# Kernel tuning notes

Measured on AMD Instinct MI355X. Metric: run time of the kernel, lower is better.

Reference implementation:

```python
import jax, jax.numpy as jnp
import numpy as np

B, L, D_MODEL, N_HEADS = 2, 2048, 2048, 16
HEAD_DIM = D_MODEL // N_HEADS
EPS = 1e-6
ROPE_THETA = 10000.0


def rms_norm(x, scale):
    # normalize over head_dim, learnable per-dim scale (QKNorm)
    var = jnp.mean(jnp.square(x), axis=-1, keepdims=True)
    return x * jax.lax.rsqrt(var + EPS) * scale


def rope(x, offset=0):
    # x: [B, H, T, D]; rotate-half rotary embedding over flattened positions
    T, D = x.shape[-2], x.shape[-1]
    half = D // 2
    inv_freq = 1.0 / (ROPE_THETA ** (jnp.arange(0, half, dtype=jnp.float32) / half))
    pos = jnp.arange(T, dtype=jnp.float32) + offset
    ang = pos[:, None] * inv_freq[None, :]            # [T, half]
    cos, sin = jnp.cos(ang), jnp.sin(ang)
    x1, x2 = x[..., :half], x[..., half:]
    return jnp.concatenate([x1 * cos - x2 * sin, x1 * sin + x2 * cos], axis=-1)


def setup_inputs() -> dict:
    key = jax.random.key(0)
    ks = jax.random.split(key, 7)
    s = 1.0 / np.sqrt(D_MODEL)
    x = jax.random.normal(ks[0], (B, L, D_MODEL), dtype=jnp.float32)
    w_qkv = jax.random.uniform(ks[1], (D_MODEL, 3 * D_MODEL), jnp.float32, -s, s)
    b_qkv = jax.random.uniform(ks[2], (3 * D_MODEL,), jnp.float32, -s, s)
    q_scale = jnp.ones((HEAD_DIM,), jnp.float32)
    k_scale = jnp.ones((HEAD_DIM,), jnp.float32)
    w_out = jax.random.uniform(ks[3], (D_MODEL, D_MODEL), jnp.float32, -s, s)
    b_out = jax.random.uniform(ks[4], (D_MODEL,), jnp.float32, -s, s)
    mask = jnp.tril(jnp.ones((L, L), dtype=bool))   # causal block mask pattern
    return {"x": x, "w_qkv": w_qkv, "b_qkv": b_qkv, "q_scale": q_scale,
            "k_scale": k_scale, "w_out": w_out, "b_out": b_out, "mask": mask}


def reference(x, w_qkv, b_qkv, q_scale, k_scale, w_out, b_out, mask):
    b, t, _ = x.shape
    qkv = x @ w_qkv + b_qkv                                   # [B, T, 3*D]
    qkv = qkv.reshape(b, t, 3, N_HEADS, HEAD_DIM)
    q, k, v = jnp.moveaxis(qkv, 2, 0)                          # each [B, T, H, D]
    q = jnp.transpose(q, (0, 2, 1, 3))                         # [B, H, T, D]
    k = jnp.transpose(k, (0, 2, 1, 3))
    v = jnp.transpose(v, (0, 2, 1, 3))
    q = rms_norm(q, q_scale)
    k = rms_norm(k, k_scale)
    q = rope(q, offset=0)
    k = rope(k, offset=0)
    scores = jnp.einsum('bhqd,bhkd->bhqk', q, k) / np.sqrt(HEAD_DIM)
    scores = jnp.where(mask[None, None, :, :], scores, jnp.float32(-1e30))
    attn = jax.nn.softmax(scores, axis=-1)
    out = jnp.einsum('bhqk,bhkd->bhqd', attn, v)               # [B, H, T, D]
    out = jnp.transpose(out, (0, 2, 1, 3)).reshape(b, t, D_MODEL)
    return out @ w_out + b_out
```

## Files before the change

### kernel.cpp

```cpp
#include <hip/hip_runtime.h>
#include <hip/hip_bf16.h>
#include <stdint.h>


typedef unsigned short ushort8 __attribute__((ext_vector_type(8)));
typedef unsigned short ushort4v __attribute__((ext_vector_type(4)));
typedef short          bf16x8 __attribute__((ext_vector_type(8)));
typedef float          f32x4  __attribute__((ext_vector_type(4)));

#define B_   2
#define L_   2048
#define DM   2048
#define NH   16
#define HD   128
#define QKW  4096

__device__ __forceinline__ uint16_t f2bf(float f){
  uint32_t u = __builtin_bit_cast(uint32_t, f);
  u += 0x7FFFu + ((u >> 16) & 1u);
  return (uint16_t)(u >> 16);
}
__device__ __forceinline__ float bf2f(uint16_t h){
  uint32_t u = ((uint32_t)h) << 16;
  return __builtin_bit_cast(float, u);
}

#define GLD16(gp, lp) __builtin_amdgcn_global_load_lds( \
  (const __attribute__((address_space(1))) void*)(gp),  \
  (__attribute__((address_space(3))) void*)(lp), 16, 0, 0)

__global__ __launch_bounds__(256) void prep(
    const float* __restrict__ Wqkv, uint16_t* __restrict__ WqkvT,
    const float* __restrict__ Wout, uint16_t* __restrict__ WoutT,
    const float* __restrict__ x, uint16_t* __restrict__ xb,
    float* __restrict__ ct, float* __restrict__ st)
{
  __shared__ float T[64][65];
  const int bid = blockIdx.x;
  const int tid = threadIdx.x;

  if (bid < 4096){
    const float* W; uint16_t* Wt; int R = 2048, C; int rb, cb;
    if (bid < 3072){ W = Wqkv; Wt = WqkvT; C = 6144; rb = bid & 31; cb = bid >> 5; }
    else           { int i = bid - 3072; W = Wout; Wt = WoutT; C = 2048; rb = i & 31; cb = i >> 5; }
#pragma unroll
    for (int i=0;i<4;i++){
      int rr = i*16 + (tid >> 4);
      int cc = (tid & 15) * 4;
      float4 v = *(const float4*)(W + (size_t)(rb*64 + rr) * C + cb*64 + cc);
      T[rr][cc] = v.x; T[rr][cc+1] = v.y; T[rr][cc+2] = v.z; T[rr][cc+3] = v.w;
    }
    __syncthreads();
    const int oc = tid >> 2, rc = (tid & 3) * 16;
    ushort8 o0, o1;
#pragma unroll
    for (int j=0;j<8;j++){ o0[j] = f2bf(T[rc+j][oc]); o1[j] = f2bf(T[rc+8+j][oc]); }
    size_t ob = (size_t)(cb*64 + oc) * R + rb*64 + rc;
    *(ushort8*)(Wt + ob)     = o0;
    *(ushort8*)(Wt + ob + 8) = o1;
  } else if (bid < 8192){
    int i = (bid - 4096) * 256 + tid;
    const float4* xv = (const float4*)x;
    float4 a = xv[(size_t)i*2], b = xv[(size_t)i*2+1];
    ushort8 v;
    v[0]=f2bf(a.x); v[1]=f2bf(a.y); v[2]=f2bf(a.z); v[3]=f2bf(a.w);
    v[4]=f2bf(b.x); v[5]=f2bf(b.y); v[6]=f2bf(b.z); v[7]=f2bf(b.w);
    *(ushort8*)(xb + (size_t)i*8) = v;
  } else {
    int i = (bid - 8192) * 256 + tid;
    int t = i >> 6, d = i & 63;
    float invf = powf(10000.f, -(float)d * (1.f/64.f));
    float s, c;
    sincosf((float)t * invf, &s, &c);
    ct[i] = c; st[i] = s;
  }
}

template<int MODE>
__global__ __launch_bounds__(512, 2) void gemm8p(
    const uint16_t* __restrict__ A, const uint16_t* __restrict__ Bt,
    const float* __restrict__ bias, void* __restrict__ Cv, void* __restrict__ Cv2,
    int M, int N, int K, int nbn, int ldc,
    const float* __restrict__ qs, const float* __restrict__ ks,
    const float* __restrict__ ct, const float* __restrict__ st)
{
  __shared__ uint16_t LA[3*16384];
  __shared__ uint16_t LB[3*8192];
  __shared__ float sums[4][2][64];
  const int nwg = (M >> 8) * nbn;
  const int q8  = nwg >> 3;
  const int id  = ((int)blockIdx.x & 7) * q8 + ((int)blockIdx.x >> 3);
  const int bm = id / nbn, bn = id % nbn;
  const int tid = threadIdx.x;
  const int lane = tid & 63, w = tid >> 6;
  const int wm = w & 3, wn = w >> 2;
  const int l15 = lane & 15, lh = lane >> 4;
  const int NT = K >> 6;

  const int qs3 = ((lane & 7) ^ ((lane >> 3) & 7)) * 8;
  const uint16_t* gA_ = A  + (size_t)((bm << 8) + (w << 5) + (lane >> 3)) * K + qs3;
  const uint16_t* gB_ = Bt + (size_t)((bn << 7) + (w << 4) + (lane >> 3)) * K + qs3;
  uint16_t* lA_ = LA + (w << 11);
  uint16_t* lB_ = LB + (w << 10);

  const int sw0 = ((lh       ^ (l15 & 7)) << 3);
  const int sw1 = (((4 | lh) ^ (l15 & 7)) << 3);
  const int aoff = (((wm << 6) + l15) << 6);
  const int boff = (((wn << 5) + l15) << 6);
  const int bno[4] = {0, 1024, 4096, 5120};

  f32x4 acc[4][4];
#pragma unroll
  for (int i=0;i<4;i++)
#pragma unroll
    for (int j=0;j<4;j++) acc[i][j] = f32x4{0.f,0.f,0.f,0.f};

  auto STAGE_A = [&](int tt, int s, int i){
    GLD16(gA_ + (size_t)tt*64 + (size_t)(i*8)*K, lA_ + s*16384 + i*512);
  };
  auto STAGE_B = [&](int tt, int s, int i){
    GLD16(gB_ + (size_t)tt*64 + (size_t)(i*8)*K, lB_ + s*8192 + i*512);
  };

#pragma unroll
  for (int i=0;i<4;i++) STAGE_A(0, 0, i);
#pragma unroll
  for (int i=0;i<2;i++) STAGE_B(0, 0, i);
#pragma unroll
  for (int i=0;i<4;i++) STAGE_A(1, 1, i);
#pragma unroll
  for (int i=0;i<2;i++) STAGE_B(1, 1, i);
  asm volatile("s_waitcnt vmcnt(6)" ::: "memory");
  __builtin_amdgcn_s_barrier();

  int sl = 0, sl2 = 2;
  for (int t = 0; t < NT; ++t){
    const bool pf = (t + 2 < NT);
    const uint16_t* la = LA + sl*16384;
    const uint16_t* lb = LB + sl*8192;

    bf16x8 af0[4], bf0[4], af1[4], bf1[4];
#pragma unroll
    for (int mi=0;mi<4;mi++) af0[mi] = *(const bf16x8*)(la + aoff + mi*1024 + sw0);
#pragma unroll
    for (int ni=0;ni<4;ni++) bf0[ni] = *(const bf16x8*)(lb + boff + bno[ni] + sw0);
#pragma unroll
    for (int mi=0;mi<4;mi++) af1[mi] = *(const bf16x8*)(la + aoff + mi*1024 + sw1);
#pragma unroll
    for (int ni=0;ni<4;ni++) bf1[ni] = *(const bf16x8*)(lb + boff + bno[ni] + sw1);
    if (pf){
      STAGE_A(t+2, sl2, 0); STAGE_A(t+2, sl2, 1);
      STAGE_A(t+2, sl2, 2); STAGE_A(t+2, sl2, 3);
      STAGE_B(t+2, sl2, 0); STAGE_B(t+2, sl2, 1);
    }
    __builtin_amdgcn_s_setprio(1);
#pragma unroll
    for (int mi=0;mi<4;mi++)
#pragma unroll
      for (int ni=0;ni<4;ni++)
        acc[mi][ni] = __builtin_amdgcn_mfma_f32_16x16x32_bf16(af0[mi], bf0[ni], acc[mi][ni], 0, 0, 0);
#pragma unroll
    for (int mi=0;mi<4;mi++)
#pragma unroll
      for (int ni=0;ni<4;ni++)
        acc[mi][ni] = __builtin_amdgcn_mfma_f32_16x16x32_bf16(af1[mi], bf1[ni], acc[mi][ni], 0, 0, 0);
    __builtin_amdgcn_s_setprio(0);

    if (t < NT-2)       { asm volatile("s_waitcnt vmcnt(6)" ::: "memory"); }
    else if (t == NT-2) { asm volatile("s_waitcnt vmcnt(0)" ::: "memory"); }
    if (t < NT-1) __builtin_amdgcn_s_barrier();
    sl  = (sl  == 2) ? 0 : sl  + 1;
    sl2 = (sl2 == 2) ? 0 : sl2 + 1;
  }

  const int cm = (bm << 8) + (wm << 6);
  const int cn = (bn << 7);
  int dc[4];
#pragma unroll
  for (int ni=0;ni<4;ni++) dc[ni] = (wn<<5) + ((ni>>1)<<6) + ((ni&1)<<4) + l15;
  float bs[4];
#pragma unroll
  for (int ni=0;ni<4;ni++) bs[ni] = bias[cn + dc[ni]];

  if (MODE == 0){
#pragma unroll
    for (int mi=0;mi<4;mi++)
#pragma unroll
      for (int r=0;r<4;r++){
        int rowg = cm + mi*16 + lh*4 + r;
#pragma unroll
        for (int ni=0;ni<4;ni++)
          ((float*)Cv)[(size_t)rowg * ldc + cn + dc[ni]] = acc[mi][ni][r] + bs[ni];
      }
  } else {
    const int part = bn >> 4;
    if (part == 2){
      uint16_t* vtp = (uint16_t*)Cv2;
      const int h  = bn & 15;
      const int bb = cm >> 11;
      const int t0 = (cm & (L_-1)) + lh*4;
#pragma unroll
      for (int mi=0;mi<4;mi++){
#pragma unroll
        for (int ni=0;ni<4;ni++){
          ushort4v pk;
#pragma unroll
          for (int r=0;r<4;r++) pk[r] = f2bf(acc[mi][ni][r] + bs[ni]);
          *(ushort4v*)(vtp + ((size_t)((bb*16 + h)*128 + dc[ni]))*L_ + t0 + mi*16) = pk;
        }
      }
    } else {
      uint16_t* Cb = (uint16_t*)Cv;
      const float* scp = part ? ks : qs;
      float scv[4];
#pragma unroll
      for (int ni=0;ni<4;ni++) scv[ni] = scp[dc[ni]];
      float ssum[4][4];
#pragma unroll
      for (int mi=0;mi<4;mi++)
#pragma unroll
        for (int r=0;r<4;r++){
          float s = 0.f;
#pragma unroll
          for (int ni=0;ni<4;ni++){
            float v = acc[mi][ni][r] + bs[ni];
            acc[mi][ni][r] = v;
            s += v*v;
          }
          s += __shfl_xor(s, 1); s += __shfl_xor(s, 2);
          s += __shfl_xor(s, 4); s += __shfl_xor(s, 8);
          ssum[mi][r] = s;
        }
      if (l15 == 0){
#pragma unroll
        for (int mi=0;mi<4;mi++)
#pragma unroll
          for (int r=0;r<4;r++) sums[wm][wn][mi*16 + lh*4 + r] = ssum[mi][r];
      }
      __syncthreads();
      const int dd0 = (wn<<5) + l15, dd1 = dd0 + 16;
#pragma unroll
      for (int mi=0;mi<4;mi++){
#pragma unroll
        for (int r=0;r<4;r++){
          int rid = mi*16 + lh*4 + r;
          float tot = ssum[mi][r] + sums[wm][wn^1][rid];
          float iv = rsqrtf(tot * 0.0078125f + 1e-6f);
          int rowg = cm + rid;
          int t = rowg & (L_-1);
          float y0 = acc[mi][0][r] * iv * scv[0];
          float y1 = acc[mi][1][r] * iv * scv[1];
          float y2 = acc[mi][2][r] * iv * scv[2];
          float y3 = acc[mi][3][r] * iv * scv[3];
          float c0 = ct[t*64 + dd0], s0 = st[t*64 + dd0];
          float c1 = ct[t*64 + dd1], s1 = st[t*64 + dd1];
          size_t rb_ = (size_t)rowg * ldc + cn;
          Cb[rb_ + dc[0]] = f2bf(y0*c0 - y2*s0);
          Cb[rb_ + dc[1]] = f2bf(y1*c1 - y3*s1);
          Cb[rb_ + dc[2]] = f2bf(y0*s0 + y2*c0);
          Cb[rb_ + dc[3]] = f2bf(y1*s1 + y3*c1);
        }
      }
    }
  }
}

__global__ __launch_bounds__(256) void flash_attn(
    const uint16_t* __restrict__ qk, const uint16_t* __restrict__ vt,
    uint16_t* __restrict__ ao)
{
  const int bh = blockIdx.x;
  const int qp = blockIdx.y;
  const int b = bh >> 4, h = bh & 15;
  const int tid = threadIdx.x;
  const int lane = tid & 63, w = tid >> 6;
  const int l15 = lane & 15, lh = lane >> 4;

  __shared__ uint16_t Ks[64][136];
  __shared__ uint16_t Vs[128][72];
  __shared__ uint16_t Ps[4][16][72];

  const float SCL = 0.12751744f;

  for (int sel = 0; sel < 2; sel++){
    const int qb = sel ? (31 - qp) : qp;

    const size_t qrow = (size_t)b * L_ + qb*64 + w*16 + l15;
    const uint16_t* qp_ = qk + qrow * QKW + h * HD;
    bf16x8 qf[4];
#pragma unroll
    for (int c = 0; c < 4; c++) qf[c] = *(const bf16x8*)(qp_ + c*32 + lh*8);

    float m_s = -3.0e38f, l_s = 0.f;
    f32x4 oacc[8];
#pragma unroll
    for (int nt = 0; nt < 8; nt++) oacc[nt] = f32x4{0.f,0.f,0.f,0.f};

    const int ntile = qb + 1;
    ushort8 rk[4], rv[4];

#pragma unroll
    for (int i = 0; i < 4; i++){
      int g = i*256 + tid, row = g >> 4, c = g & 15;
      rk[i] = *(const ushort8*)(qk + ((size_t)b*L_ + row)*QKW + DM + h*HD + c*8);
    }
#pragma unroll
    for (int i = 0; i < 4; i++){
      int g = i*256 + tid, d = g >> 3, c = g & 7;
      rv[i] = *(const ushort8*)(vt + ((size_t)bh*HD + d)*L_ + c*8);
    }

    for (int kt = 0; kt < ntile; kt++){
      __syncthreads();
#pragma unroll
      for (int i = 0; i < 4; i++){ int g = i*256+tid; *(ushort8*)(&Ks[g>>4][(g&15)*8]) = rk[i]; }
#pragma unroll
      for (int i = 0; i < 4; i++){ int g = i*256+tid; *(ushort8*)(&Vs[g>>3][(g&7)*8]) = rv[i]; }
      __syncthreads();

      if (kt + 1 < ntile){
        const int k2 = (kt + 1) * 64;
#pragma unroll
        for (int i = 0; i < 4; i++){
          int g = i*256 + tid, row = g >> 4, c = g & 15;
          rk[i] = *(const ushort8*)(qk + ((size_t)b*L_ + k2 + row)*QKW + DM + h*HD + c*8);
        }
#pragma unroll
        for (int i = 0; i < 4; i++){
          int g = i*256 + tid, d = g >> 3, c = g & 7;
          rv[i] = *(const ushort8*)(vt + ((size_t)bh*HD + d)*L_ + k2 + c*8);
        }
      }

      f32x4 s[4];
#pragma unroll
      for (int nt = 0; nt < 4; nt++) s[nt] = f32x4{0.f,0.f,0.f,0.f};
      __builtin_amdgcn_s_setprio(1);
#pragma unroll
      for (int c = 0; c < 4; c++){
#pragma unroll
        for (int nt = 0; nt < 4; nt++){
          bf16x8 kf = *(const bf16x8*)(&Ks[nt*16 + l15][c*32 + lh*8]);
          s[nt] = __builtin_amdgcn_mfma_f32_16x16x32_bf16(kf, qf[c], s[nt], 0, 0, 0);
        }
      }
      __builtin_amdgcn_s_setprio(0);

      const bool diag = (kt == qb);
      const int qg = w*16 + l15;
      const int kb = lh*4;
#pragma unroll
      for (int nt = 0; nt < 4; nt++){
#pragma unroll
        for (int r = 0; r < 4; r++){
          float v = s[nt][r] * SCL;
          if (diag && (nt*16 + kb + r > qg)) v = -1.0e30f;
          s[nt][r] = v;
        }
      }
      float pm = s[0][0];
#pragma unroll
      for (int nt = 0; nt < 4; nt++)
#pragma unroll
        for (int r = 0; r < 4; r++) pm = fmaxf(pm, s[nt][r]);
      pm = fmaxf(pm, __shfl_xor(pm, 16));
      pm = fmaxf(pm, __shfl_xor(pm, 32));
      if (!__all(pm - m_s <= 8.0f)){
        float mn = fmaxf(m_s, pm);
        float alpha = exp2f(m_s - mn);
        m_s = mn; l_s *= alpha;
        float ar[4];
#pragma unroll
        for (int r = 0; r < 4; r++) ar[r] = __shfl(alpha, lh*4 + r);
#pragma unroll
        for (int nt = 0; nt < 8; nt++)
#pragma unroll
          for (int r = 0; r < 4; r++) oacc[nt][r] *= ar[r];
      }
      float rs = 0.f;
#pragma unroll
      for (int nt = 0; nt < 4; nt++){
        float p0 = exp2f(s[nt][0] - m_s);
        float p1 = exp2f(s[nt][1] - m_s);
        float p2 = exp2f(s[nt][2] - m_s);
        float p3 = exp2f(s[nt][3] - m_s);
        rs += (p0 + p1) + (p2 + p3);
        uint2 pk;
        pk.x = (uint32_t)f2bf(p0) | ((uint32_t)f2bf(p1) << 16);
        pk.y = (uint32_t)f2bf(p2) | ((uint32_t)f2bf(p3) << 16);
        *(uint2*)(&Ps[w][l15][nt*16 + kb]) = pk;
      }
      rs += __shfl_xor(rs, 16);
      rs += __shfl_xor(rs, 32);
      l_s += rs;

      asm volatile("s_waitcnt lgkmcnt(0)" ::: "memory");
      __builtin_amdgcn_s_setprio(1);
#pragma unroll
      for (int kc = 0; kc < 2; kc++){
        bf16x8 pf = *(const bf16x8*)(&Ps[w][l15][kc*32 + lh*8]);
#pragma unroll
        for (int nt = 0; nt < 8; nt++){
          bf16x8 vf = *(const bf16x8*)(&Vs[nt*16 + l15][kc*32 + lh*8]);
          oacc[nt] = __builtin_amdgcn_mfma_f32_16x16x32_bf16(pf, vf, oacc[nt], 0, 0, 0);
        }
      }
      __builtin_amdgcn_s_setprio(0);
    }
    float invl[4];
#pragma unroll
    for (int r = 0; r < 4; r++) invl[r] = 1.f / __shfl(l_s, lh*4 + r);
#pragma unroll
    for (int nt = 0; nt < 8; nt++){
#pragma unroll
      for (int r = 0; r < 4; r++){
        float v = oacc[nt][r] * invl[r];
        size_t row = (size_t)b*L_ + qb*64 + w*16 + lh*4 + r;
        ao[row * DM + h*HD + nt*16 + l15] = f2bf(v);
      }
    }
  }
}

extern "C" void kernel_launch(void* const* d_in, const int* in_sizes, int n_in,
                              void* d_out, int out_size, void* d_ws, size_t ws_size,
                              hipStream_t stream)
{
  (void)in_sizes; (void)n_in; (void)out_size; (void)ws_size;
  const float* x       = (const float*)d_in[0];
  const float* w_qkv   = (const float*)d_in[1];
  const float* b_qkv   = (const float*)d_in[2];
  const float* q_scale = (const float*)d_in[3];
  const float* k_scale = (const float*)d_in[4];
  const float* w_out   = (const float*)d_in[5];
  const float* b_out   = (const float*)d_in[6];
  float* out = (float*)d_out;

  char* ws = (char*)d_ws;
  uint16_t* qk    = (uint16_t*)(ws);
  uint16_t* vt    = (uint16_t*)(ws + 33554432);
  uint16_t* reg1  = (uint16_t*)(ws + 50331648);
  uint16_t* wqkvT = (uint16_t*)(ws + 67108864);
  uint16_t* woutT = (uint16_t*)(ws + 92274688);
  float*    ct    = (float*)(ws + 100663296);
  float*    st    = ct + 131072;

  uint16_t* xb = reg1;
  uint16_t* ao = reg1;

  prep        <<<8704, 256, 0, stream>>>(w_qkv, wqkvT, w_out, woutT, x, xb, ct, st);
  gemm8p<1>   <<<768, 512, 0, stream>>>(xb, wqkvT, b_qkv, qk, vt,
                                        4096, 6144, 2048, 48, 4096,
                                        q_scale, k_scale, ct, st);
  flash_attn  <<<dim3(32, 16), 256, 0, stream>>>(qk, vt, ao);
  gemm8p<0>   <<<256, 512, 0, stream>>>(ao, woutT, b_out, out, nullptr,
                                        4096, 2048, 2048, 16, 2048,
                                        nullptr, nullptr, nullptr, nullptr);
}
```

Measured before the change: 248.3 us.

## Use 256x256 tiles with split-phase double-buffered pipeline for QKV GEMM

Replaces the templated QKV projection GEMM with a dedicated kernel using 256x256 output tiles (8x4 MFMA fragments per wave), a two-stage LDS buffer and a four-phase inner loop. Prefetches are interleaved between MFMA groups, and some waves issue next-tile A loads early. The bigger tile raises arithmetic intensity and halves the grid from 768 to 384 workgroups, but adds register pressure and more barriers. The output GEMM is simplified to a plain non-template epilogue with contiguous column mapping.

```diff
diff --git a/kernel.cpp b/kernel.cpp
--- a/kernel.cpp
+++ b/kernel.cpp
@@ -76,17 +76,207 @@
   }
 }
 
-template<int MODE>
-__global__ __launch_bounds__(512, 2) void gemm8p(
+__global__ __launch_bounds__(512, 2) void gemm256q(
     const uint16_t* __restrict__ A, const uint16_t* __restrict__ Bt,
-    const float* __restrict__ bias, void* __restrict__ Cv, void* __restrict__ Cv2,
-    int M, int N, int K, int nbn, int ldc,
+    const float* __restrict__ bias, uint16_t* __restrict__ qkOut,
+    uint16_t* __restrict__ vtOut,
     const float* __restrict__ qs, const float* __restrict__ ks,
     const float* __restrict__ ct, const float* __restrict__ st)
 {
+  constexpr int K = 2048, NT = 32, nbn = 24;
+  __shared__ uint16_t LA[2*16384];
+  __shared__ uint16_t LB[2*16384];
+  __shared__ float sums[2][4][128];
+  const int q8 = 48;
+  const int id = ((int)blockIdx.x & 7) * q8 + ((int)blockIdx.x >> 3);
+  const int bm = id / nbn, bn = id % nbn;
+  const int tid = threadIdx.x;
+  const int lane = tid & 63, w = tid >> 6;
+  const int wm = w >> 2, wn = w & 3;
+  const int l15 = lane & 15, lh = lane >> 4;
+  const bool g1 = ((w & 2) == 0);
+
+  const int qs3 = ((lane & 7) ^ ((lane >> 3) & 7)) * 8;
+  const uint16_t* gA_ = A  + (size_t)(bm*256 + w*32 + (lane >> 3)) * K + qs3;
+  const uint16_t* gB_ = Bt + (size_t)(bn*256 + w*32 + (lane >> 3)) * K + qs3;
+
+  const int sw0 = ((lh       ^ (l15 & 7)) << 3);
+  const int sw1 = (((4 | lh) ^ (l15 & 7)) << 3);
+  const int aoff = ((wm*128 + l15) << 6);
+  const int cbase = ((wn >> 1) << 7) + ((wn & 1) << 5);
+  const int boff = ((cbase + l15) << 6);
+  const int bno[4] = {0, 1024, 4096, 5120};
+
+  f32x4 acc[8][4];
+#pragma unroll
+  for (int i=0;i<8;i++)
+#pragma unroll
+    for (int j=0;j<4;j++) acc[i][j] = f32x4{0.f,0.f,0.f,0.f};
+
+  auto SA = [&](int tt, int i){
+    GLD16(gA_ + (size_t)tt*64 + (size_t)(i*8)*K, LA + ((tt&1)<<14) + w*2048 + i*512);
+  };
+  auto SB = [&](int tt, int i){
+    GLD16(gB_ + (size_t)tt*64 + (size_t)(i*8)*K, LB + ((tt&1)<<14) + w*2048 + i*512);
+  };
+
+#pragma unroll
+  for (int i=0;i<4;i++) SA(0, i);
+#pragma unroll
+  for (int i=0;i<4;i++) SB(0, i);
+#pragma unroll
+  for (int i=0;i<4;i++) SA(1, i);
+#pragma unroll
+  for (int i=0;i<4;i++) SB(1, i);
+  asm volatile("s_waitcnt vmcnt(8)" ::: "memory");
+  __builtin_amdgcn_s_barrier();
+
+  for (int t = 0; t < NT; ++t){
+    const uint16_t* la = LA + ((t&1) << 14);
+    const uint16_t* lb = LB + ((t&1) << 14);
+    bf16x8 af[4], bk0[4], bk1[4];
+    const bool sY = (!g1) && (t >= 1) && (t+1 < NT);
+    const bool s2 = (t+2 < NT);
+
+#pragma unroll
+    for (int j=0;j<4;j++) af[j] = *(const bf16x8*)(la + aoff + j*1024 + sw0);
+#pragma unroll
+    for (int ni=0;ni<4;ni++) bk0[ni] = *(const bf16x8*)(lb + boff + bno[ni] + sw0);
+    if (sY){ SA(t+1, 0); SA(t+1, 1); }
+    __builtin_amdgcn_s_setprio(1);
+#pragma unroll
+    for (int j=0;j<4;j++)
+#pragma unroll
+      for (int ni=0;ni<4;ni++)
+        acc[j][ni] = __builtin_amdgcn_mfma_f32_16x16x32_bf16(af[j], bk0[ni], acc[j][ni], 0, 0, 0);
+    __builtin_amdgcn_s_setprio(0);
+    __builtin_amdgcn_s_barrier();
+
+#pragma unroll
+    for (int j=0;j<4;j++) af[j] = *(const bf16x8*)(la + aoff + j*1024 + sw1);
+#pragma unroll
+    for (int ni=0;ni<4;ni++) bk1[ni] = *(const bf16x8*)(lb + boff + bno[ni] + sw1);
+    if (sY){ SA(t+1, 2); SA(t+1, 3); }
+    __builtin_amdgcn_s_setprio(1);
+#pragma unroll
+    for (int j=0;j<4;j++)
+#pragma unroll
+      for (int ni=0;ni<4;ni++)
+        acc[j][ni] = __builtin_amdgcn_mfma_f32_16x16x32_bf16(af[j], bk1[ni], acc[j][ni], 0, 0, 0);
+    __builtin_amdgcn_s_setprio(0);
+    __builtin_amdgcn_s_barrier();
+
+#pragma unroll
+    for (int j=0;j<4;j++) af[j] = *(const bf16x8*)(la + aoff + (4+j)*1024 + sw0);
+    if (s2){ if (g1){ SA(t+2, 0); SA(t+2, 1); } SB(t+2, 0); SB(t+2, 1); }
+    __builtin_amdgcn_s_setprio(1);
+#pragma unroll
+    for (int j=0;j<4;j++)
+#pragma unroll
+      for (int ni=0;ni<4;ni++)
+        acc[4+j][ni] = __builtin_amdgcn_mfma_f32_16x16x32_bf16(af[j], bk0[ni], acc[4+j][ni], 0, 0, 0);
+    __builtin_amdgcn_s_setprio(0);
+    __builtin_amdgcn_s_barrier();
+
+#pragma unroll
+    for (int j=0;j<4;j++) af[j] = *(const bf16x8*)(la + aoff + (4+j)*1024 + sw1);
+    if (s2){ if (g1){ SA(t+2, 2); SA(t+2, 3); } SB(t+2, 2); SB(t+2, 3); }
+    __builtin_amdgcn_s_setprio(1);
+#pragma unroll
+    for (int j=0;j<4;j++)
+#pragma unroll
+      for (int ni=0;ni<4;ni++)
+        acc[4+j][ni] = __builtin_amdgcn_mfma_f32_16x16x32_bf16(af[j], bk1[ni], acc[4+j][ni], 0, 0, 0);
+    __builtin_amdgcn_s_setprio(0);
+    if (t == NT-2)     { asm volatile("s_waitcnt vmcnt(0)" ::: "memory"); }
+    else if (t < NT-2) { asm volatile("s_waitcnt vmcnt(4)" ::: "memory"); }
+    if (t < NT-1) __builtin_amdgcn_s_barrier();
+  }
+
+  const int cmBase = bm*256 + wm*128;
+  int dc[4];
+#pragma unroll
+  for (int ni=0;ni<4;ni++) dc[ni] = cbase + ((ni>>1)<<6) + ((ni&1)<<4) + l15;
+  float bs[4];
+#pragma unroll
+  for (int ni=0;ni<4;ni++) bs[ni] = bias[bn*256 + dc[ni]];
+
+  const int part = bn >> 3;
+  if (part == 2){
+    const int h  = ((bn & 7) << 1) + (wn >> 1);
+    const int bb = bm >> 3;
+    const int t0 = (cmBase & (L_-1)) + lh*4;
+#pragma unroll
+    for (int mi=0;mi<8;mi++){
+#pragma unroll
+      for (int ni=0;ni<4;ni++){
+        ushort4v pk;
+#pragma unroll
+        for (int r=0;r<4;r++) pk[r] = f2bf(acc[mi][ni][r] + bs[ni]);
+        *(ushort4v*)(vtOut + ((size_t)((bb*16 + h)*128 + (dc[ni] & 127)))*L_ + t0 + mi*16) = pk;
+      }
+    }
+  } else {
+    const float* scp = part ? ks : qs;
+    float scv[4];
+#pragma unroll
+    for (int ni=0;ni<4;ni++) scv[ni] = scp[dc[ni] & 127];
+    float ssum[8][4];
+#pragma unroll
+    for (int mi=0;mi<8;mi++)
+#pragma unroll
+      for (int r=0;r<4;r++){
+        float s = 0.f;
+#pragma unroll
+        for (int ni=0;ni<4;ni++){
+          float v = acc[mi][ni][r] + bs[ni];
+          acc[mi][ni][r] = v;
+          s += v*v;
+        }
+        s += __shfl_xor(s, 1); s += __shfl_xor(s, 2);
+        s += __shfl_xor(s, 4); s += __shfl_xor(s, 8);
+        ssum[mi][r] = s;
+      }
+    if (l15 == 0){
+#pragma unroll
+      for (int mi=0;mi<8;mi++)
+#pragma unroll
+        for (int r=0;r<4;r++) sums[wm][wn][mi*16 + lh*4 + r] = ssum[mi][r];
+    }
+    __syncthreads();
+    const int dd0 = ((wn & 1) << 5) + l15, dd1 = dd0 + 16;
+#pragma unroll
+    for (int mi=0;mi<8;mi++){
+#pragma unroll
+      for (int r=0;r<4;r++){
+        int rid = mi*16 + lh*4 + r;
+        float tot = ssum[mi][r] + sums[wm][wn^1][rid];
+        float iv = rsqrtf(tot * 0.0078125f + 1e-6f);
+        int rowg = cmBase + rid;
+        int tt = rowg & (L_-1);
+        float y0 = acc[mi][0][r] * iv * scv[0];
+        float y1 = acc[mi][1][r] * iv * scv[1];
+        float y2 = acc[mi][2][r] * iv * scv[2];
+        float y3 = acc[mi][3][r] * iv * scv[3];
+        float c0 = ct[tt*64 + dd0], s0 = st[tt*64 + dd0];
+        float c1 = ct[tt*64 + dd1], s1 = st[tt*64 + dd1];
+        size_t rb_ = (size_t)rowg * QKW + bn*256;
+        qkOut[rb_ + dc[0]] = f2bf(y0*c0 - y2*s0);
+        qkOut[rb_ + dc[1]] = f2bf(y1*c1 - y3*s1);
+        qkOut[rb_ + dc[2]] = f2bf(y0*s0 + y2*c0);
+        qkOut[rb_ + dc[3]] = f2bf(y1*s1 + y3*c1);
+      }
+    }
+  }
+}
+
+__global__ __launch_bounds__(512, 2) void gemm8p(
+    const uint16_t* __restrict__ A, const uint16_t* __restrict__ Bt,
+    const float* __restrict__ bias, float* __restrict__ Cv,
+    int M, int N, int K, int nbn)
+{
   __shared__ uint16_t LA[3*16384];
   __shared__ uint16_t LB[3*8192];
-  __shared__ float sums[4][2][64];
   const int nwg = (M >> 8) * nbn;
   const int q8  = nwg >> 3;
   const int id  = ((int)blockIdx.x & 7) * q8 + ((int)blockIdx.x >> 3);
@@ -106,8 +296,7 @@
   const int sw0 = ((lh       ^ (l15 & 7)) << 3);
   const int sw1 = (((4 | lh) ^ (l15 & 7)) << 3);
   const int aoff = (((wm << 6) + l15) << 6);
-  const int boff = (((wn << 5) + l15) << 6);
-  const int bno[4] = {0, 1024, 4096, 5120};
+  const int boff = (((wn << 6) + l15) << 6);
 
   f32x4 acc[4][4];
 #pragma unroll
@@ -143,11 +332,11 @@
 #pragma unroll
     for (int mi=0;mi<4;mi++) af0[mi] = *(const bf16x8*)(la + aoff + mi*1024 + sw0);
 #pragma unroll
-    for (int ni=0;ni<4;ni++) bf0[ni] = *(const bf16x8*)(lb + boff + bno[ni] + sw0);
+    for (int ni=0;ni<4;ni++) bf0[ni] = *(const bf16x8*)(lb + boff + ni*1024 + sw0);
 #pragma unroll
     for (int mi=0;mi<4;mi++) af1[mi] = *(const bf16x8*)(la + aoff + mi*1024 + sw1);
 #pragma unroll
-    for (int ni=0;ni<4;ni++) bf1[ni] = *(const bf16x8*)(lb + boff + bno[ni] + sw1);
+    for (int ni=0;ni<4;ni++) bf1[ni] = *(const bf16x8*)(lb + boff + ni*1024 + sw1);
     if (pf){
       STAGE_A(t+2, sl2, 0); STAGE_A(t+2, sl2, 1);
       STAGE_A(t+2, sl2, 2); STAGE_A(t+2, sl2, 3);
@@ -174,92 +363,17 @@
   }
 
   const int cm = (bm << 8) + (wm << 6);
-  const int cn = (bn << 7);
-  int dc[4];
-#pragma unroll
-  for (int ni=0;ni<4;ni++) dc[ni] = (wn<<5) + ((ni>>1)<<6) + ((ni&1)<<4) + l15;
-  float bs[4];
-#pragma unroll
-  for (int ni=0;ni<4;ni++) bs[ni] = bias[cn + dc[ni]];
-
-  if (MODE == 0){
-#pragma unroll
-    for (int mi=0;mi<4;mi++)
+  const int cn = (bn << 7) + (wn << 6);
+#pragma unroll
+  for (int ni=0;ni<4;ni++){
+    int col = cn + ni*16 + l15;
+    float bsv = bias[col];
+#pragma unroll
+    for (int mi=0;mi<4;mi++){
 #pragma unroll
       for (int r=0;r<4;r++){
         int rowg = cm + mi*16 + lh*4 + r;
-#pragma unroll
-        for (int ni=0;ni<4;ni++)
-          ((float*)Cv)[(size_t)rowg * ldc + cn + dc[ni]] = acc[mi][ni][r] + bs[ni];
-      }
-  } else {
-    const int part = bn >> 4;
-    if (part == 2){
-      uint16_t* vtp = (uint16_t*)Cv2;
-      const int h  = bn & 15;
-      const int bb = cm >> 11;
-      const int t0 = (cm & (L_-1)) + lh*4;
-#pragma unroll
-      for (int mi=0;mi<4;mi++){
-#pragma unroll
-        for (int ni=0;ni<4;ni++){
-          ushort4v pk;
-#pragma unroll
-          for (int r=0;r<4;r++) pk[r] = f2bf(acc[mi][ni][r] + bs[ni]);
-          *(ushort4v*)(vtp + ((size_t)((bb*16 + h)*128 + dc[ni]))*L_ + t0 + mi*16) = pk;
-        }
-      }
-    } else {
-      uint16_t* Cb = (uint16_t*)Cv;
-      const float* scp = part ? ks : qs;
-      float scv[4];
-#pragma unroll
-      for (int ni=0;ni<4;ni++) scv[ni] = scp[dc[ni]];
-      float ssum[4][4];
-#pragma unroll
-      for (int mi=0;mi<4;mi++)
-#pragma unroll
-        for (int r=0;r<4;r++){
-          float s = 0.f;
-#pragma unroll
-          for (int ni=0;ni<4;ni++){
-            float v = acc[mi][ni][r] + bs[ni];
-            acc[mi][ni][r] = v;
-            s += v*v;
-          }
-          s += __shfl_xor(s, 1); s += __shfl_xor(s, 2);
-          s += __shfl_xor(s, 4); s += __shfl_xor(s, 8);
-          ssum[mi][r] = s;
-        }
-      if (l15 == 0){
-#pragma unroll
-        for (int mi=0;mi<4;mi++)
-#pragma unroll
-          for (int r=0;r<4;r++) sums[wm][wn][mi*16 + lh*4 + r] = ssum[mi][r];
-      }
-      __syncthreads();
-      const int dd0 = (wn<<5) + l15, dd1 = dd0 + 16;
-#pragma unroll
-      for (int mi=0;mi<4;mi++){
-#pragma unroll
-        for (int r=0;r<4;r++){
-          int rid = mi*16 + lh*4 + r;
-          float tot = ssum[mi][r] + sums[wm][wn^1][rid];
-          float iv = rsqrtf(tot * 0.0078125f + 1e-6f);
-          int rowg = cm + rid;
-          int t = rowg & (L_-1);
-          float y0 = acc[mi][0][r] * iv * scv[0];
-          float y1 = acc[mi][1][r] * iv * scv[1];
-          float y2 = acc[mi][2][r] * iv * scv[2];
-          float y3 = acc[mi][3][r] * iv * scv[3];
-          float c0 = ct[t*64 + dd0], s0 = st[t*64 + dd0];
-          float c1 = ct[t*64 + dd1], s1 = st[t*64 + dd1];
-          size_t rb_ = (size_t)rowg * ldc + cn;
-          Cb[rb_ + dc[0]] = f2bf(y0*c0 - y2*s0);
-          Cb[rb_ + dc[1]] = f2bf(y1*c1 - y3*s1);
-          Cb[rb_ + dc[2]] = f2bf(y0*s0 + y2*c0);
-          Cb[rb_ + dc[3]] = f2bf(y1*s1 + y3*c1);
-        }
+        Cv[(size_t)rowg * N + col] = acc[mi][ni][r] + bsv;
       }
     }
   }
@@ -449,11 +563,8 @@
   uint16_t* ao = reg1;
 
   prep        <<<8704, 256, 0, stream>>>(w_qkv, wqkvT, w_out, woutT, x, xb, ct, st);
-  gemm8p<1>   <<<768, 512, 0, stream>>>(xb, wqkvT, b_qkv, qk, vt,
-                                        4096, 6144, 2048, 48, 4096,
+  gemm256q    <<<384, 512, 0, stream>>>(xb, wqkvT, b_qkv, qk, vt,
                                         q_scale, k_scale, ct, st);
   flash_attn  <<<dim3(32, 16), 256, 0, stream>>>(qk, vt, ao);
-  gemm8p<0>   <<<256, 512, 0, stream>>>(ao, woutT, b_out, out, nullptr,
-                                        4096, 2048, 2048, 16, 2048,
-                                        nullptr, nullptr, nullptr, nullptr);
-}
+  gemm8p      <<<256, 512, 0, stream>>>(ao, woutT, b_out, out, 4096, 2048, 2048, 16);
+}
```

Result: slower. 267.3 us (+7.7%).
